# Kernel optimization log

Measured on AMD Instinct MI355X. Metric: run time of the kernel, lower is better.

Reference implementation:

```python
import jax, jax.numpy as jnp
import numpy as np

N = 50000      # nodes
E = 800000     # edges
D_IN = 128     # embedding_in
EP = 200000    # prediction edge pairs
CONV_DIMS = [D_IN, 128, 64, 32]
LIN_DIMS = [32, 16, 8, 1]


def setup_inputs() -> dict:
    key = jax.random.key(0)
    ks = jax.random.split(key, 20)
    inp = {
        "x": jax.random.normal(ks[0], (N, D_IN), dtype=jnp.float32),
        "edge_index": jax.random.randint(ks[1], (2, E), 0, N, dtype=jnp.int64 if jax.config.jax_enable_x64 else jnp.int32),
        "pred_edges": jax.random.randint(ks[2], (EP, 2), 0, N, dtype=jnp.int64 if jax.config.jax_enable_x64 else jnp.int32),
    }
    k = 3
    for i in range(3):  # GCNConv weights [in,out] + bias (torch GCNConv has bias)
        din, dout = CONV_DIMS[i], CONV_DIMS[i + 1]
        inp[f"cw{i}"] = jax.random.normal(ks[k], (din, dout), dtype=jnp.float32) / np.sqrt(din); k += 1
        inp[f"cb{i}"] = jax.random.normal(ks[k], (dout,), dtype=jnp.float32) * 0.01; k += 1
    for i in range(3):  # Linear weights stored [in,out]
        din, dout = LIN_DIMS[i], LIN_DIMS[i + 1]
        inp[f"lw{i}"] = jax.random.normal(ks[k], (din, dout), dtype=jnp.float32) / np.sqrt(din); k += 1
        inp[f"lb{i}"] = jax.random.normal(ks[k], (dout,), dtype=jnp.float32) * 0.01; k += 1
    return inp


def gcn_conv(x, W, b, src, dst, n):
    """PyG GCNConv: D^-1/2 (A + I) D^-1/2 X W + b, deg over dst incl. self-loop."""
    h = x @ W  # [n, dout]
    deg = jax.ops.segment_sum(jnp.ones_like(dst, dtype=h.dtype), dst, num_segments=n) + 1.0
    dis = jax.lax.rsqrt(deg)  # deg >= 1 (self loop)
    msg = h[src] * (dis[src] * dis[dst])[:, None]      # gather + per-edge normalize
    out = jax.ops.segment_sum(msg, dst, num_segments=n)  # scatter-add into targets
    out = out + h * (dis * dis)[:, None]                # self-loop contribution
    return out + b


def reference(x, edge_index, pred_edges, cw0, cb0, cw1, cb1, cw2, cb2,
              lw0, lb0, lw1, lb1, lw2, lb2):
    src, dst = edge_index[0], edge_index[1]
    n = x.shape[0]
    for W, b in ((cw0, cb0), (cw1, cb1), (cw2, cb2)):
        x = jax.nn.relu(gcn_conv(x, W, b, src, dst, n))
    x = jax.nn.relu(x @ lw0 + lb0)
    x = jax.nn.relu(x @ lw1 + lb1)
    x = jax.nn.sigmoid(x @ lw2 + lb2)  # [n, 1]
    s = x[:, 0]
    # x[pred_edges] -> [EP,2,1]; mul of pair, transpose+flatten -> [EP]
    return s[pred_edges[:, 0]] * s[pred_edges[:, 1]]
```

## Files before the change

kernel.cpp:

```cpp
#include <hip/hip_runtime.h>
#include <math.h>

constexpr int NN  = 50000;
constexpr int NP  = 50048;
constexpr int NE  = 800000;
constexpr int NEP = 200000;

constexpr int NBKT  = 256;
constexpr int CAP   = 4096;
constexpr int CAPC  = 4096;
constexpr int CHUNK = 4096;

constexpr int BKB = (NE + CHUNK - 1) / CHUNK;
constexpr int W0B = 128 * 128 / 256;
constexpr int W1B = 128 * 64 / 256;
constexpr int W2B = 64 * 32 / 256;
constexpr int FRONT_BLOCKS = BKB + W0B + W1B + W2B;

constexpr int GEMM0_BLKS = NP / 64;
constexpr int NODE_BLKS32 = (NN + 31) / 32;
constexpr int NODE_BLKS16 = (NN + 15) / 16;

typedef _Float16 half8_t  __attribute__((ext_vector_type(8)));
typedef __fp16   fp16x2_t __attribute__((ext_vector_type(2)));
typedef float    float4_t __attribute__((ext_vector_type(4)));

static inline int cdiv(long long a, int b) { return (int)((a + b - 1) / b); }

__global__ __launch_bounds__(256) void k_front(const int* __restrict__ src,
        const int* __restrict__ dst, int* __restrict__ binCnt,
        unsigned int* __restrict__ ebuf,
        const float* __restrict__ cw0, _Float16* __restrict__ WT0,
        const float* __restrict__ cw1, _Float16* __restrict__ WT1,
        const float* __restrict__ cw2, _Float16* __restrict__ WT2) {
    const int tid = threadIdx.x;
    const int bid = blockIdx.x;

    if (bid < BKB) {
        __shared__ int hist[NBKT];
        __shared__ int base[NBKT];
        __shared__ int cur[NBKT];
        constexpr int J = CHUNK / 256;
        const int e0 = bid * CHUNK;
        hist[tid] = 0;
        __syncthreads();
        int  s[J], bn[J], dl[J];
        bool ok[J];
#pragma unroll
        for (int j = 0; j < J; ++j) {
            int i = e0 + j * 256 + tid;
            ok[j] = i < NE;
            if (ok[j]) {
                int d = dst[i];
                s[j]  = src[i];
                bn[j] = d >> 8;
                dl[j] = d & 255;
                atomicAdd(&hist[bn[j]], 1);
            }
        }
        __syncthreads();
        base[tid] = hist[tid] ? atomicAdd(&binCnt[tid], hist[tid]) : 0;
        cur[tid] = 0;
        __syncthreads();
#pragma unroll
        for (int j = 0; j < J; ++j) {
            if (ok[j]) {
                int slot = base[bn[j]] + atomicAdd(&cur[bn[j]], 1);
                ebuf[bn[j] * CAP + slot] = (unsigned int)s[j] | ((unsigned int)dl[j] << 16);
            }
        }
        return;
    }
    if (bid < BKB + W0B) {
        int idx = (bid - BKB) * 256 + tid;
        int k = idx >> 7, n = idx & 127;
        WT0[(size_t)n * 128 + k] = (_Float16)cw0[idx];
        return;
    }
    if (bid < BKB + W0B + W1B) {
        int idx = (bid - BKB - W0B) * 256 + tid;
        int k = idx >> 6, n = idx & 63;
        WT1[(size_t)n * 128 + k] = (_Float16)cw1[idx];
        return;
    }
    {
        int idx = (bid - BKB - W0B - W1B) * 256 + tid;
        int k = idx >> 5, n = idx & 31;
        WT2[(size_t)n * 64 + k] = (_Float16)cw2[idx];
    }
}

__global__ __launch_bounds__(256) void k_csr_gemm0(const unsigned int* __restrict__ ebuf,
        const int* __restrict__ binCnt, int* __restrict__ off, float* __restrict__ dis,
        unsigned short* __restrict__ csr,
        const float* __restrict__ X, const _Float16* __restrict__ WT,
        _Float16* __restrict__ g, int n) {
    const int tid = threadIdx.x;
    const int bid = blockIdx.x;

    if (bid < NBKT) {
        __shared__ int hist[256];
        __shared__ int sh[256];
        __shared__ int cur[256];
        const int bin = bid;
        const int cnt = binCnt[bin];
        const unsigned int* eb = ebuf + (size_t)bin * CAP;

        hist[tid] = 0;
        __syncthreads();
        for (int i = tid; i < cnt; i += 256)
            atomicAdd(&hist[eb[i] >> 16], 1);
        __syncthreads();

        int v  = hist[tid];
        int pv = (v + 3) & ~3;
        sh[tid] = pv;
        __syncthreads();
        for (int d = 1; d < 256; d <<= 1) {
            int t = (tid >= d) ? sh[tid - d] : 0;
            __syncthreads();
            sh[tid] += t;
            __syncthreads();
        }
        int start = bin * CAPC + (sh[tid] - pv);

        int node = bin * 256 + tid;
        if (node < NN) {
            off[node] = start | (pv << 20);
            dis[node] = rsqrtf((float)v + 1.0f);
        } else if (node == NN) {
            dis[node] = 0.f;
        }
        cur[tid] = start;
        __syncthreads();

        for (int i = tid; i < cnt; i += 256) {
            unsigned int e = eb[i];
            int p = atomicAdd(&cur[e >> 16], 1);
            csr[p] = (unsigned short)(e & 0xFFFFu);
        }
        for (int k2 = v; k2 < pv; ++k2) csr[start + k2] = (unsigned short)NN;
        return;
    }

    constexpr int K = 128, DOUT = 128;
    constexpr int NC = 64, NT = 4, KT = 4, MT = 2;

    const int gb   = bid - NBKT;
    const int L    = tid & 63;
    const int w    = tid >> 6;
    const int wc   = w & 1;
    const int wr   = w >> 1;
    const int r0   = gb * 64 + wr * 32;
    const int c0   = wc * NC;
    const int quad = L >> 4;
    const int lm   = L & 15;

    float4_t acc[MT][NT];
#pragma unroll
    for (int mt = 0; mt < MT; ++mt)
#pragma unroll
        for (int nt = 0; nt < NT; ++nt) acc[mt][nt] = (float4_t){0.f, 0.f, 0.f, 0.f};

#pragma unroll
    for (int kt = 0; kt < KT; ++kt) {
        half8_t a[MT], b[NT];
#pragma unroll
        for (int mt = 0; mt < MT; ++mt) {
            const float* xr = X + (size_t)(r0 + mt * 16 + lm) * K + kt * 32 + quad * 8;
            float4 u = *(const float4*)xr;
            float4 v = *(const float4*)(xr + 4);
            union { fp16x2_t h2[4]; half8_t h8; } cv;
            cv.h2[0] = __builtin_amdgcn_cvt_pkrtz(u.x, u.y);
            cv.h2[1] = __builtin_amdgcn_cvt_pkrtz(u.z, u.w);
            cv.h2[2] = __builtin_amdgcn_cvt_pkrtz(v.x, v.y);
            cv.h2[3] = __builtin_amdgcn_cvt_pkrtz(v.z, v.w);
            a[mt] = cv.h8;
        }
#pragma unroll
        for (int nt = 0; nt < NT; ++nt)
            b[nt] = *(const half8_t*)(WT + (size_t)(c0 + nt * 16 + lm) * K + kt * 32 + quad * 8);
#pragma unroll
        for (int mt = 0; mt < MT; ++mt)
#pragma unroll
            for (int nt = 0; nt < NT; ++nt)
                acc[mt][nt] = __builtin_amdgcn_mfma_f32_16x16x32_f16(a[mt], b[nt], acc[mt][nt], 0, 0, 0);
    }

#pragma unroll
    for (int mt = 0; mt < MT; ++mt) {
        int rb = r0 + mt * 16 + quad * 4;
#pragma unroll
        for (int nt = 0; nt < NT; ++nt) {
            int c = c0 + nt * 16 + lm;
#pragma unroll
            for (int reg = 0; reg < 4; ++reg) {
                int r = rb + reg;
                if (r < n)       g[(size_t)r * DOUT + c] = (_Float16)acc[mt][nt][reg];
                else if (r == n) g[(size_t)r * DOUT + c] = (_Float16)0.f;
            }
        }
    }
}

__global__ __launch_bounds__(256) void k_agg_gemm16(const half8_t* __restrict__ gin,
        const float* __restrict__ dis, const float* __restrict__ bias,
        const int* __restrict__ off, const unsigned short* __restrict__ csr,
        const _Float16* __restrict__ WT, _Float16* __restrict__ gout, int n) {
    constexpr int DIN = 128, DOUT = 64;
    constexpr int R8 = DIN / 8;
    constexpr int XS = DIN + 8;
    __shared__ _Float16 sX[16 * XS];

    const int tid  = threadIdx.x;
    const int l16  = tid & 15;
    const int ln   = tid >> 4;
    const int r0   = blockIdx.x * 16;
    const int node = r0 + ln;

    if (blockIdx.x == 0 && tid < DOUT / 8)
        ((half8_t*)(gout + (size_t)n * DOUT))[tid] =
            (half8_t){(_Float16)0.f, (_Float16)0.f, (_Float16)0.f, (_Float16)0.f,
                      (_Float16)0.f, (_Float16)0.f, (_Float16)0.f, (_Float16)0.f};

    float dd = dis[node];
    half8_t hv = gin[(size_t)node * R8 + l16];
    float a[8];
#pragma unroll
    for (int j = 0; j < 8; ++j) a[j] = dd * (float)hv[j];

    int pk = off[node];
    int e0 = pk & 0xFFFFF;
    int e1 = e0 + (pk >> 20);
    int e = e0;
    for (; e + 7 < e1; e += 8) {
        ushort4 c4 = *(const ushort4*)(csr + e);
        ushort4 c8 = *(const ushort4*)(csr + e + 4);
        half8_t v0 = gin[(size_t)c4.x * R8 + l16];
        half8_t v1 = gin[(size_t)c4.y * R8 + l16];
        half8_t v2 = gin[(size_t)c4.z * R8 + l16];
        half8_t v3 = gin[(size_t)c4.w * R8 + l16];
        half8_t v4 = gin[(size_t)c8.x * R8 + l16];
        half8_t v5 = gin[(size_t)c8.y * R8 + l16];
        half8_t v6 = gin[(size_t)c8.z * R8 + l16];
        half8_t v7 = gin[(size_t)c8.w * R8 + l16];
        float d0 = dis[c4.x], d1 = dis[c4.y], d2 = dis[c4.z], d3 = dis[c4.w];
        float d4 = dis[c8.x], d5 = dis[c8.y], d6 = dis[c8.z], d7 = dis[c8.w];
#pragma unroll
        for (int j = 0; j < 8; ++j)
            a[j] = fmaf((float)v7[j], d7,
                   fmaf((float)v6[j], d6,
                   fmaf((float)v5[j], d5,
                   fmaf((float)v4[j], d4,
                   fmaf((float)v3[j], d3,
                   fmaf((float)v2[j], d2,
                   fmaf((float)v1[j], d1,
                   fmaf((float)v0[j], d0, a[j]))))))));
    }
    if (e < e1) {
        ushort4 c4 = *(const ushort4*)(csr + e);
        half8_t v0 = gin[(size_t)c4.x * R8 + l16];
        half8_t v1 = gin[(size_t)c4.y * R8 + l16];
        half8_t v2 = gin[(size_t)c4.z * R8 + l16];
        half8_t v3 = gin[(size_t)c4.w * R8 + l16];
        float d0 = dis[c4.x], d1 = dis[c4.y], d2 = dis[c4.z], d3 = dis[c4.w];
#pragma unroll
        for (int j = 0; j < 8; ++j)
            a[j] = fmaf((float)v3[j], d3,
                   fmaf((float)v2[j], d2,
                   fmaf((float)v1[j], d1,
                   fmaf((float)v0[j], d0, a[j]))));
    }
    {
        half8_t o;
#pragma unroll
        for (int j = 0; j < 8; ++j)
            o[j] = (_Float16)fmaxf(fmaf(a[j], dd, bias[l16 * 8 + j]), 0.f);
        *(half8_t*)(sX + ln * XS + l16 * 8) = o;
    }
    __syncthreads();

    const int L    = tid & 63;
    const int w    = tid >> 6;
    const int quad = L >> 4;
    const int lm   = L & 15;
    const int c0   = w * 16;

    float4_t acc = (float4_t){0.f, 0.f, 0.f, 0.f};
#pragma unroll
    for (int kt = 0; kt < DIN / 32; ++kt) {
        half8_t b  = *(const half8_t*)(WT + (size_t)(c0 + lm) * DIN + kt * 32 + quad * 8);
        half8_t aF = *(const half8_t*)(sX + lm * XS + kt * 32 + quad * 8);
        acc = __builtin_amdgcn_mfma_f32_16x16x32_f16(aF, b, acc, 0, 0, 0);
    }
    int rb = r0 + quad * 4;
    float dv[4];
    *(float4*)dv = *(const float4*)(dis + rb);
#pragma unroll
    for (int reg = 0; reg < 4; ++reg)
        gout[(size_t)(rb + reg) * DOUT + c0 + lm] = (_Float16)(acc[reg] * dv[reg]);
}

__global__ __launch_bounds__(256) void k_agg_gemm8(const half8_t* __restrict__ gin,
        const float* __restrict__ dis, const float* __restrict__ bias,
        const int* __restrict__ off, const unsigned short* __restrict__ csr,
        const _Float16* __restrict__ WT, _Float16* __restrict__ gout, int n) {
    constexpr int DIN = 64, DOUT = 32;
    constexpr int R8 = DIN / 8;
    constexpr int XS = DIN + 8;
    __shared__ _Float16 sX[32 * XS];

    const int tid  = threadIdx.x;
    const int l8   = tid & 7;
    const int ln   = tid >> 3;
    const int r0   = blockIdx.x * 32;
    const int node = r0 + ln;

    if (node < n) {
        float dd = dis[node];
        half8_t hv = gin[(size_t)node * R8 + l8];
        float a[8];
#pragma unroll
        for (int j = 0; j < 8; ++j) a[j] = (float)hv[j];
        int pk = off[node];
        int e0 = pk & 0xFFFFF;
        int e1 = e0 + (pk >> 20);
        int e = e0;
        for (; e + 7 < e1; e += 8) {
            ushort4 c4 = *(const ushort4*)(csr + e);
            ushort4 c8 = *(const ushort4*)(csr + e + 4);
            half8_t v0 = gin[(size_t)c4.x * R8 + l8];
            half8_t v1 = gin[(size_t)c4.y * R8 + l8];
            half8_t v2 = gin[(size_t)c4.z * R8 + l8];
            half8_t v3 = gin[(size_t)c4.w * R8 + l8];
            half8_t v4 = gin[(size_t)c8.x * R8 + l8];
            half8_t v5 = gin[(size_t)c8.y * R8 + l8];
            half8_t v6 = gin[(size_t)c8.z * R8 + l8];
            half8_t v7 = gin[(size_t)c8.w * R8 + l8];
#pragma unroll
            for (int j = 0; j < 8; ++j)
                a[j] += ((float)v0[j] + (float)v1[j]) + ((float)v2[j] + (float)v3[j])
                      + ((float)v4[j] + (float)v5[j]) + ((float)v6[j] + (float)v7[j]);
        }
        if (e < e1) {
            ushort4 c4 = *(const ushort4*)(csr + e);
            half8_t v0 = gin[(size_t)c4.x * R8 + l8];
            half8_t v1 = gin[(size_t)c4.y * R8 + l8];
            half8_t v2 = gin[(size_t)c4.z * R8 + l8];
            half8_t v3 = gin[(size_t)c4.w * R8 + l8];
#pragma unroll
            for (int j = 0; j < 8; ++j)
                a[j] += ((float)v0[j] + (float)v1[j]) + ((float)v2[j] + (float)v3[j]);
        }
        half8_t o;
#pragma unroll
        for (int j = 0; j < 8; ++j)
            o[j] = (_Float16)fmaxf(fmaf(a[j], dd, bias[l8 * 8 + j]), 0.f);
        *(half8_t*)(sX + ln * XS + l8 * 8) = o;
    } else {
        *(half8_t*)(sX + ln * XS + l8 * 8) =
            (half8_t){(_Float16)0.f, (_Float16)0.f, (_Float16)0.f, (_Float16)0.f,
                      (_Float16)0.f, (_Float16)0.f, (_Float16)0.f, (_Float16)0.f};
    }
    __syncthreads();

    const int L    = tid & 63;
    const int w    = tid >> 6;
    const int quad = L >> 4;
    const int lm   = L & 15;
    const int c0   = (w & 1) * 16;
    const int m0   = (w >> 1) * 16;

    float4_t acc = (float4_t){0.f, 0.f, 0.f, 0.f};
#pragma unroll
    for (int kt = 0; kt < DIN / 32; ++kt) {
        half8_t b  = *(const half8_t*)(WT + (size_t)(c0 + lm) * DIN + kt * 32 + quad * 8);
        half8_t aF = *(const half8_t*)(sX + (m0 + lm) * XS + kt * 32 + quad * 8);
        acc = __builtin_amdgcn_mfma_f32_16x16x32_f16(aF, b, acc, 0, 0, 0);
    }
    int rb = r0 + m0 + quad * 4;
    float dv[4];
    *(float4*)dv = *(const float4*)(dis + rb);
#pragma unroll
    for (int reg = 0; reg < 4; ++reg) {
        int r = rb + reg;
        if (r < n)       gout[(size_t)r * DOUT + c0 + lm] = (_Float16)(acc[reg] * dv[reg]);
        else if (r == n) gout[(size_t)r * DOUT + c0 + lm] = (_Float16)0.f;
    }
}

__global__ __launch_bounds__(256) void k_agg_mlp(const half8_t* __restrict__ g,
        const float* __restrict__ dis, const float* __restrict__ b,
        const int* __restrict__ off, const unsigned short* __restrict__ csr,
        const float* __restrict__ lw0, const float* __restrict__ lb0,
        const float* __restrict__ lw1, const float* __restrict__ lb1,
        const float* __restrict__ lw2, const float* __restrict__ lb2,
        float* __restrict__ sv, int n) {
    __shared__ float sh[32 * 33];
    const int tid  = threadIdx.x;
    const int l8   = tid & 7;
    const int lane = l8 & 3;
    const int grp  = l8 >> 2;
    const int ln   = tid >> 3;
    const int node = blockIdx.x * 32 + ln;

    if (node < n) {
        float dd = dis[node];
        half8_t hv = g[(size_t)node * 4 + lane];
        float a[8];
#pragma unroll
        for (int j = 0; j < 8; ++j) a[j] = (grp == 0) ? (float)hv[j] : 0.f;
        int pk = off[node];
        int e0 = pk & 0xFFFFF;
        int e1 = e0 + (pk >> 20);
        for (int e = e0 + grp * 4; e < e1; e += 8) {
            ushort4 c4 = *(const ushort4*)(csr + e);
            half8_t v0 = g[(size_t)c4.x * 4 + lane];
            half8_t v1 = g[(size_t)c4.y * 4 + lane];
            half8_t v2 = g[(size_t)c4.z * 4 + lane];
            half8_t v3 = g[(size_t)c4.w * 4 + lane];
#pragma unroll
            for (int j = 0; j < 8; ++j)
                a[j] += (float)v0[j] + (float)v1[j] + (float)v2[j] + (float)v3[j];
        }
#pragma unroll
        for (int j = 0; j < 8; ++j) a[j] += __shfl_xor(a[j], 4);
        if (grp == 0) {
            float* row = sh + ln * 33 + lane * 8;
#pragma unroll
            for (int j = 0; j < 8; ++j)
                row[j] = fmaxf(fmaf(a[j], dd, b[lane * 8 + j]), 0.f);
        }
    }
    __syncthreads();

    if (tid < 32) {
        int node2 = blockIdx.x * 32 + tid;
        if (node2 < n) {
            const float* v = sh + tid * 33;
            float a[16];
#pragma unroll
            for (int j = 0; j < 16; ++j) {
                float acc = lb0[j];
#pragma unroll
                for (int k = 0; k < 32; ++k) acc = fmaf(v[k], lw0[k * 16 + j], acc);
                a[j] = fmaxf(acc, 0.f);
            }
            float b8[8];
#pragma unroll
            for (int j = 0; j < 8; ++j) {
                float acc = lb1[j];
#pragma unroll
                for (int k = 0; k < 16; ++k) acc = fmaf(a[k], lw1[k * 8 + j], acc);
                b8[j] = fmaxf(acc, 0.f);
            }
            float z = lb2[0];
#pragma unroll
            for (int k = 0; k < 8; ++k) z = fmaf(b8[k], lw2[k], z);
            sv[node2] = 1.0f / (1.0f + expf(-z));
        }
    }
}

__global__ void k_pred(const float* __restrict__ s, const int* __restrict__ pe,
                       float* __restrict__ out, int ep2) {
    int i = blockIdx.x * blockDim.x + threadIdx.x;
    if (i >= ep2) return;
    int4 p = ((const int4*)pe)[i];
    float2 o;
    o.x = s[p.x] * s[p.y];
    o.y = s[p.z] * s[p.w];
    ((float2*)out)[i] = o;
}

extern "C" void kernel_launch(void* const* d_in, const int* in_sizes, int n_in,
                              void* d_out, int out_size, void* d_ws, size_t ws_size,
                              hipStream_t stream) {
    const float* x   = (const float*)d_in[0];
    const int*   ei  = (const int*)d_in[1];
    const int*   pe  = (const int*)d_in[2];
    const float* cw0 = (const float*)d_in[3];
    const float* cb0 = (const float*)d_in[4];
    const float* cw1 = (const float*)d_in[5];
    const float* cb1 = (const float*)d_in[6];
    const float* cw2 = (const float*)d_in[7];
    const float* cb2 = (const float*)d_in[8];
    const float* lw0 = (const float*)d_in[9];
    const float* lb0 = (const float*)d_in[10];
    const float* lw1 = (const float*)d_in[11];
    const float* lb1 = (const float*)d_in[12];
    const float* lw2 = (const float*)d_in[13];
    const float* lb2 = (const float*)d_in[14];

    const int* src = ei;
    const int* dst = ei + NE;

    char* w = (char*)d_ws;
    float*          dis  = (float*)w;           w += sizeof(float) * (NN + 16);
    _Float16*       M0   = (_Float16*)w;        w += sizeof(_Float16) * (size_t)(NN + 1) * 128;
    _Float16*       M1   = (_Float16*)w;        w += sizeof(_Float16) * (size_t)(NN + 1) * 64;
    _Float16*       M2   = (_Float16*)w;        w += sizeof(_Float16) * (size_t)(NN + 1) * 32;
    float*          sv   = (float*)w;           w += sizeof(float) * NN;
    _Float16*       WT0  = (_Float16*)w;        w += sizeof(_Float16) * 128 * 128;
    _Float16*       WT1  = (_Float16*)w;        w += sizeof(_Float16) * 64 * 128;
    _Float16*       WT2  = (_Float16*)w;        w += sizeof(_Float16) * 32 * 64;
    int*            off  = (int*)w;             w += sizeof(int) * NN;
    unsigned short* csr  = (unsigned short*)w;  w += sizeof(unsigned short) * (size_t)NBKT * CAPC;
    int*            binCnt = (int*)w;           w += sizeof(int) * NBKT;
    unsigned int*   ebuf = (unsigned int*)w;    w += sizeof(unsigned int) * (size_t)NBKT * CAP;

    const int T = 256;

    (void)hipMemsetAsync(binCnt, 0, sizeof(int) * NBKT, stream);
    k_front<<<FRONT_BLOCKS, 256, 0, stream>>>(src, dst, binCnt, ebuf,
                                              cw0, WT0, cw1, WT1, cw2, WT2);

    k_csr_gemm0<<<NBKT + GEMM0_BLKS, 256, 0, stream>>>(ebuf, binCnt, off, dis, csr,
                                                       x, WT0, M0, NN);

    k_agg_gemm16<<<NODE_BLKS16, 256, 0, stream>>>((const half8_t*)M0, dis, cb0,
                                                  off, csr, WT1, M1, NN);

    k_agg_gemm8<<<NODE_BLKS32, 256, 0, stream>>>((const half8_t*)M1, dis, cb1,
                                                 off, csr, WT2, M2, NN);

    k_agg_mlp<<<NODE_BLKS32, 256, 0, stream>>>((const half8_t*)M2, dis, cb2, off, csr,
                                               lw0, lb0, lw1, lb1, lw2, lb2, sv, NN);

    k_pred<<<cdiv(NEP / 2, T), T, 0, stream>>>(sv, pe, (float*)d_out, NEP / 2);
}
```

Baseline: 199.1 us.

## Prescale layer-0 features by source inverse sqrt degree to drop per-edge dis loads

Adds a global per-node degree histogram via atomics in the front kernel, so the first GEMM epilogue can scale each output row by rsqrt(deg+1) before storing. The first aggregation kernel then sums prescaled neighbor rows directly, removing the per-edge gather of dis and the multiplies. This costs 800k extra global atomics and a larger memset in exchange for fewer scattered loads in the aggregation loop. Only layer 0 is changed, and the fp16 storage of the prescaled values changes rounding slightly.

```diff
diff --git a/kernel.cpp b/kernel.cpp
--- a/kernel.cpp
+++ b/kernel.cpp
@@ -29,7 +29,7 @@
 
 __global__ __launch_bounds__(256) void k_front(const int* __restrict__ src,
         const int* __restrict__ dst, int* __restrict__ binCnt,
-        unsigned int* __restrict__ ebuf,
+        unsigned int* __restrict__ ebuf, int* __restrict__ deg,
         const float* __restrict__ cw0, _Float16* __restrict__ WT0,
         const float* __restrict__ cw1, _Float16* __restrict__ WT1,
         const float* __restrict__ cw2, _Float16* __restrict__ WT2) {
@@ -56,6 +56,7 @@
                 bn[j] = d >> 8;
                 dl[j] = d & 255;
                 atomicAdd(&hist[bn[j]], 1);
+                atomicAdd(&deg[d], 1);
             }
         }
         __syncthreads();
@@ -92,7 +93,7 @@
 
 __global__ __launch_bounds__(256) void k_csr_gemm0(const unsigned int* __restrict__ ebuf,
         const int* __restrict__ binCnt, int* __restrict__ off, float* __restrict__ dis,
-        unsigned short* __restrict__ csr,
+        unsigned short* __restrict__ csr, const int* __restrict__ deg,
         const float* __restrict__ X, const _Float16* __restrict__ WT,
         _Float16* __restrict__ g, int n) {
     const int tid = threadIdx.x;
@@ -190,13 +191,19 @@
 #pragma unroll
     for (int mt = 0; mt < MT; ++mt) {
         int rb = r0 + mt * 16 + quad * 4;
+        int4 d4 = *(const int4*)(deg + rb);
+        float dv[4];
+        dv[0] = rsqrtf((float)d4.x + 1.0f);
+        dv[1] = rsqrtf((float)d4.y + 1.0f);
+        dv[2] = rsqrtf((float)d4.z + 1.0f);
+        dv[3] = rsqrtf((float)d4.w + 1.0f);
 #pragma unroll
         for (int nt = 0; nt < NT; ++nt) {
             int c = c0 + nt * 16 + lm;
 #pragma unroll
             for (int reg = 0; reg < 4; ++reg) {
                 int r = rb + reg;
-                if (r < n)       g[(size_t)r * DOUT + c] = (_Float16)acc[mt][nt][reg];
+                if (r < n)       g[(size_t)r * DOUT + c] = (_Float16)(acc[mt][nt][reg] * dv[reg]);
                 else if (r == n) g[(size_t)r * DOUT + c] = (_Float16)0.f;
             }
         }
@@ -227,7 +234,7 @@
     half8_t hv = gin[(size_t)node * R8 + l16];
     float a[8];
 #pragma unroll
-    for (int j = 0; j < 8; ++j) a[j] = dd * (float)hv[j];
+    for (int j = 0; j < 8; ++j) a[j] = (float)hv[j];
 
     int pk = off[node];
     int e0 = pk & 0xFFFFF;
@@ -244,18 +251,10 @@
         half8_t v5 = gin[(size_t)c8.y * R8 + l16];
         half8_t v6 = gin[(size_t)c8.z * R8 + l16];
         half8_t v7 = gin[(size_t)c8.w * R8 + l16];
-        float d0 = dis[c4.x], d1 = dis[c4.y], d2 = dis[c4.z], d3 = dis[c4.w];
-        float d4 = dis[c8.x], d5 = dis[c8.y], d6 = dis[c8.z], d7 = dis[c8.w];
 #pragma unroll
         for (int j = 0; j < 8; ++j)
-            a[j] = fmaf((float)v7[j], d7,
-                   fmaf((float)v6[j], d6,
-                   fmaf((float)v5[j], d5,
-                   fmaf((float)v4[j], d4,
-                   fmaf((float)v3[j], d3,
-                   fmaf((float)v2[j], d2,
-                   fmaf((float)v1[j], d1,
-                   fmaf((float)v0[j], d0, a[j]))))))));
+            a[j] += ((float)v0[j] + (float)v1[j]) + ((float)v2[j] + (float)v3[j])
+                  + ((float)v4[j] + (float)v5[j]) + ((float)v6[j] + (float)v7[j]);
     }
     if (e < e1) {
         ushort4 c4 = *(const ushort4*)(csr + e);
@@ -263,13 +262,9 @@
         half8_t v1 = gin[(size_t)c4.y * R8 + l16];
         half8_t v2 = gin[(size_t)c4.z * R8 + l16];
         half8_t v3 = gin[(size_t)c4.w * R8 + l16];
-        float d0 = dis[c4.x], d1 = dis[c4.y], d2 = dis[c4.z], d3 = dis[c4.w];
 #pragma unroll
         for (int j = 0; j < 8; ++j)
-            a[j] = fmaf((float)v3[j], d3,
-                   fmaf((float)v2[j], d2,
-                   fmaf((float)v1[j], d1,
-                   fmaf((float)v0[j], d0, a[j]))));
+            a[j] += ((float)v0[j] + (float)v1[j]) + ((float)v2[j] + (float)v3[j]);
     }
     {
         half8_t o;
@@ -507,16 +502,17 @@
     int*            off  = (int*)w;             w += sizeof(int) * NN;
     unsigned short* csr  = (unsigned short*)w;  w += sizeof(unsigned short) * (size_t)NBKT * CAPC;
     int*            binCnt = (int*)w;           w += sizeof(int) * NBKT;
+    int*            deg  = (int*)w;             w += sizeof(int) * NP;
     unsigned int*   ebuf = (unsigned int*)w;    w += sizeof(unsigned int) * (size_t)NBKT * CAP;
 
     const int T = 256;
 
-    (void)hipMemsetAsync(binCnt, 0, sizeof(int) * NBKT, stream);
-    k_front<<<FRONT_BLOCKS, 256, 0, stream>>>(src, dst, binCnt, ebuf,
+    (void)hipMemsetAsync(binCnt, 0, sizeof(int) * (NBKT + NP), stream);
+    k_front<<<FRONT_BLOCKS, 256, 0, stream>>>(src, dst, binCnt, ebuf, deg,
                                               cw0, WT0, cw1, WT1, cw2, WT2);
 
     k_csr_gemm0<<<NBKT + GEMM0_BLKS, 256, 0, stream>>>(ebuf, binCnt, off, dis, csr,
-                                                       x, WT0, M0, NN);
+                                                       deg, x, WT0, M0, NN);
 
     k_agg_gemm16<<<NODE_BLKS16, 256, 0, stream>>>((const half8_t*)M0, dis, cb0,
                                                   off, csr, WT1, M1, NN);
```

Measured after the change: 224.1 us. 12.5% more time.
